# Optimization experiments

Hardware: AMD Instinct MI355X
Metric: run time of the kernel (lower is better)

## Reference

```python
import jax, jax.numpy as jnp
import numpy as np

N_ADAPTERS = 8
RANK = 64  # per-adapter LoRA rank (uniform here; ragged in general)
SCALINGS = np.full((N_ADAPTERS,), 2.0, dtype=np.float32)  # alpha / r


def setup_inputs() -> dict:
    key = jax.random.key(0)
    k1, k2, k3, k4, k5 = jax.random.split(key, 5)
    T, DIN, DOUT = 8192, 4096, 4096
    total_rank = N_ADAPTERS * RANK
    x = jax.random.normal(k1, (T, DIN), dtype=jnp.float32)
    lora_A = jax.random.normal(k2, (total_rank, DIN), dtype=jnp.float32) * 0.02
    lora_B = jax.random.normal(k3, (total_rank, DOUT), dtype=jnp.float32) * 0.02
    base_output = jax.random.normal(k4, (T, DOUT), dtype=jnp.float32)
    adapter_ids = jax.random.randint(k5, (T,), 0, N_ADAPTERS, dtype=jnp.int64)
    return {"x": x, "lora_A": lora_A, "lora_B": lora_B,
            "base_output": base_output, "adapter_ids": adapter_ids}


def reference(x, lora_A, lora_B, base_output, adapter_ids):
    """Multi-adapter LoRA: out = base + scaling[a] * (x @ A_a.T) @ B_a per token.

    base_slice covers the full out_features here, so the LoRA delta is added
    to the whole base_output. Loop is over the small fixed adapter set.
    """
    lora_out = jnp.zeros_like(base_output)
    for a in range(N_ADAPTERS):
        A_a = lora_A[a * RANK:(a + 1) * RANK]  # [R, DIN]
        B_a = lora_B[a * RANK:(a + 1) * RANK]  # [R, DOUT]
        xa = x @ A_a.T                          # [T, R]
        mask = (adapter_ids == a).astype(x.dtype)[:, None]
        lora_out = lora_out + SCALINGS[a] * ((xa * mask) @ B_a)
    return base_output + lora_out
```

## Files before the change

### kernel.cpp

```cpp
#include <hip/hip_runtime.h>
#include <hip/hip_bf16.h>

#define T_TOK 8192
#define DIN   4096
#define DOUT  4096
#define RANK  64
#define NAD   8
#define TS    32
#define MAXTILES 264
#define TOTR  (NAD*RANK)
#define KSPLIT 4
#define KCH   (DIN / KSPLIT)
#define NT    (KCH / 64)
#define DSPLIT 8
#define DCH   (DOUT / DSPLIT)
#define NS    (DCH / 64)

typedef __bf16 bf16x8 __attribute__((ext_vector_type(8)));
typedef __bf16 bf16x4 __attribute__((ext_vector_type(4)));
typedef float  f32x4  __attribute__((ext_vector_type(4)));

#define WS_CURSORS 0
#define WS_NTILES  64
#define WS_FLAG    128
#define WS_TINFO   256
#define WS_PERM    4096
#define WS_XA      0x10000
#define WS_ABF     0x110000
#define WS_BT      0x510000
#define WS_XAP     0x910000
#define WS_END     (0x910000 + (size_t)KSPLIT * T_TOK * RANK * 4)

__device__ __forceinline__ void gll16(const void* g, void* l) {
  __builtin_amdgcn_global_load_lds(
      (const __attribute__((address_space(1))) unsigned int*)g,
      (__attribute__((address_space(3))) unsigned int*)l, 16, 0, 0);
}

__global__ __launch_bounds__(1024) void hist_prep(const int* __restrict__ ids,
    int* __restrict__ cursors, int* __restrict__ ntilesp,
    int* __restrict__ flagp, int* __restrict__ tinfo) {
  __shared__ int cnt[NAD];
  __shared__ int s_ofs[NAD], s_tbase[NAD + 1];
  __shared__ int s_is64;
  int tid = threadIdx.x, lane = tid & 63;
  if (tid < NAD) cnt[tid] = 0;
  if (tid == 0) s_is64 = 1;
  __syncthreads();
  int any = 0;
  for (int i = tid; i < T_TOK; i += 1024)
    if (i & 1) any |= ids[i];
  if (any) s_is64 = 0;
  __syncthreads();
  int is64 = s_is64;
  int loc[NAD];
#pragma unroll
  for (int a = 0; a < NAD; ++a) loc[a] = 0;
  for (int t = tid; t < T_TOK; t += 1024) {
    int id = (is64 ? ids[2 * t] : ids[t]) & 7;
#pragma unroll
    for (int a = 0; a < NAD; ++a) {
      unsigned long long m = __ballot(id == a);
      if (lane == 0) loc[a] += __popcll(m);
    }
  }
  if (lane == 0) {
#pragma unroll
    for (int a = 0; a < NAD; ++a) if (loc[a]) atomicAdd(&cnt[a], loc[a]);
  }
  __syncthreads();
  if (tid == 0) {
    *flagp = is64;
    int ofs = 0, tb = 0;
    for (int a = 0; a < NAD; ++a) {
      s_ofs[a] = ofs; cursors[a] = ofs;
      s_tbase[a] = tb;
      ofs += cnt[a];
      tb += (cnt[a] + TS - 1) / TS;
    }
    s_tbase[NAD] = tb;
    *ntilesp = tb;
  }
  __syncthreads();
  int ntt = s_tbase[NAD];
  for (int e = tid; e < ntt; e += 1024) {
    int a = 0;
    while (e >= s_tbase[a + 1]) ++a;
    int t0 = (e - s_tbase[a]) * TS;
    int c = cnt[a];
    tinfo[e * 3 + 0] = a;
    tinfo[e * 3 + 1] = s_ofs[a] + t0;
    tinfo[e * 3 + 2] = (c - t0 < TS) ? (c - t0) : TS;
  }
}

__global__ __launch_bounds__(256) void scatter_k(const int* __restrict__ ids,
    const int* __restrict__ flagp, int* __restrict__ cursors, int* __restrict__ perm) {
  int t = blockIdx.x * 256 + threadIdx.x;
  int lane = threadIdx.x & 63;
  int id = ((*flagp) ? ids[2 * t] : ids[t]) & 7;
  unsigned long long lt = (1ull << lane) - 1ull;
#pragma unroll
  for (int a = 0; a < NAD; ++a) {
    unsigned long long m = __ballot(id == a);
    if (m) {
      int leader = __ffsll((long long)m) - 1;
      int base_a = 0;
      if (lane == leader) base_a = atomicAdd(&cursors[a], __popcll(m));
      base_a = __shfl(base_a, leader, 64);
      if (id == a) perm[base_a + __popcll(m & lt)] = t;
    }
  }
}

__global__ __launch_bounds__(256) void prep_ab(const float* __restrict__ A,
    __bf16* __restrict__ Abf, const float* __restrict__ B, __bf16* __restrict__ Bt) {
  if (blockIdx.x < 2048) {
    int i = blockIdx.x * 256 + threadIdx.x;
    float4 v = ((const float4*)A)[i];
    bf16x4 o = { (__bf16)v.x, (__bf16)v.y, (__bf16)v.z, (__bf16)v.w };
    ((bf16x4*)Abf)[i] = o;
  } else {
    __shared__ float t[64][65];
    int idx = blockIdx.x - 2048;
    int rb = idx & 7, db = idx >> 3;
    int tid = threadIdx.x;
    int c = tid & 63, q = tid >> 6;
#pragma unroll
    for (int i = 0; i < 16; ++i) {
      int r = i * 4 + q;
      t[r][c] = B[(size_t)(rb * 64 + r) * DOUT + db * 64 + c];
    }
    __syncthreads();
#pragma unroll
    for (int i = 0; i < 16; ++i) {
      int d = i * 4 + q;
      Bt[(size_t)(db * 64 + d) * TOTR + rb * 64 + c] = (__bf16)t[c][d];
    }
  }
}

#define CVT8(lo, hi) { (__bf16)lo.x, (__bf16)lo.y, (__bf16)lo.z, (__bf16)lo.w, \
                       (__bf16)hi.x, (__bf16)hi.y, (__bf16)hi.z, (__bf16)hi.w }

__global__ __launch_bounds__(512) void stage1s(const float* __restrict__ x,
    const __bf16* __restrict__ Abf, const int* __restrict__ tinfo,
    const int* __restrict__ ntilesp, const int* __restrict__ perm,
    float* __restrict__ xap) {
  __shared__ char lds[4][16384];
  int b = blockIdx.x;
  if (b >= *ntilesp) return;
  int ks = blockIdx.y;
  int a = tinfo[b * 3], start = tinfo[b * 3 + 1], nv = tinfo[b * 3 + 2];
  int tid = threadIdx.x, lane = tid & 63, wv = tid >> 6;

  int xr = wv * 4 + (lane >> 4);
  int xtok = (xr < nv) ? perm[start + xr] : perm[start];
  int xinner = ((lane & 15) * 16) ^ ((xr & 7) << 4);
  const char* xsrc = (const char*)(x + (size_t)xtok * DIN + ks * KCH) + xinner;
  int ar = wv * 8 + (lane >> 3);
  int ainner = ((lane & 7) * 16) ^ ((ar & 7) << 4);
  const char* asrc = (const char*)(Abf + (size_t)(a * RANK + ar) * DIN + ks * KCH) + ainner;

  int l16 = lane & 15, lq = lane >> 4;
  int rb = wv & 1, cb = wv >> 1;
  int xrow = rb * 16 + l16;
  int arow = cb * 16 + l16;
  int swx = (xrow & 7) << 4;
  int swa = (arow & 7) << 4;

  f32x4 acc = {0.f, 0.f, 0.f, 0.f};

#pragma unroll
  for (int p = 0; p < 3; ++p) {
    gll16(xsrc + (size_t)p * 256, &lds[p][wv * 1024]);
    gll16(asrc + (size_t)p * 128, &lds[p][8192 + wv * 1024]);
  }

  for (int t = 0; t < NT; ++t) {
    if (t < NT - 2)       asm volatile("s_waitcnt vmcnt(4)" ::: "memory");
    else if (t == NT - 2) asm volatile("s_waitcnt vmcnt(2)" ::: "memory");
    else                  asm volatile("s_waitcnt vmcnt(0)" ::: "memory");
    __builtin_amdgcn_s_barrier();
    asm volatile("" ::: "memory");
    if (t + 3 < NT) {
      char* nbuf = lds[(t + 3) & 3];
      gll16(xsrc + (size_t)(t + 3) * 256, nbuf + wv * 1024);
      gll16(asrc + (size_t)(t + 3) * 128, nbuf + 8192 + wv * 1024);
    }
    const char* cbuf = lds[t & 3];
#pragma unroll
    for (int m = 0; m < 2; ++m) {
      f32x4 xv0 = *(const f32x4*)(cbuf + xrow * 256 + ((m * 128 + lq * 32) ^ swx));
      f32x4 xv1 = *(const f32x4*)(cbuf + xrow * 256 + ((m * 128 + lq * 32 + 16) ^ swx));
      bf16x8 xf = { (__bf16)xv0[0], (__bf16)xv0[1], (__bf16)xv0[2], (__bf16)xv0[3],
                    (__bf16)xv1[0], (__bf16)xv1[1], (__bf16)xv1[2], (__bf16)xv1[3] };
      bf16x8 af = *(const bf16x8*)(cbuf + 8192 + arow * 128 + ((m * 64 + lq * 16) ^ swa));
      acc = __builtin_amdgcn_mfma_f32_16x16x32_bf16(xf, af, acc, 0, 0, 0);
    }
    asm volatile("" ::: "memory");
  }

  float* xo = xap + (size_t)ks * T_TOK * RANK;
#pragma unroll
  for (int j = 0; j < 4; ++j) {
    int tr = rb * 16 + lq * 4 + j;
    if (tr < nv) {
      int tk = perm[start + tr];
      xo[(size_t)tk * RANK + cb * 16 + l16] = acc[j];
    }
  }
}

__global__ __launch_bounds__(256) void reduce_xa(const float* __restrict__ xap,
                                                 __bf16* __restrict__ xa) {
  int i = blockIdx.x * 256 + threadIdx.x;
  const float4* p = (const float4*)xap;
  float4 s = p[i];
#pragma unroll
  for (int ks = 1; ks < KSPLIT; ++ks) {
    float4 q = p[(size_t)ks * (T_TOK * RANK / 4) + i];
    s.x += q.x; s.y += q.y; s.z += q.z; s.w += q.w;
  }
  bf16x4 o = { (__bf16)s.x, (__bf16)s.y, (__bf16)s.z, (__bf16)s.w };
  ((bf16x4*)xa)[i] = o;
}

__global__ __launch_bounds__(512) void stage1f(const float* __restrict__ x,
    const __bf16* __restrict__ Abf, const int* __restrict__ tinfo,
    const int* __restrict__ ntilesp, const int* __restrict__ perm,
    __bf16* __restrict__ xa) {
  int b = blockIdx.x;
  if (b >= *ntilesp) return;
  int a = tinfo[b * 3], start = tinfo[b * 3 + 1], nv = tinfo[b * 3 + 2];
  int tid = threadIdx.x, lane = tid & 63, w = tid >> 6;
  int rb = w & 1, cb = w >> 1;
  int l16 = lane & 15, lq = lane >> 4;
  int trow = rb * 16 + l16;
  int tok = (trow < nv) ? perm[start + trow] : 0;
  const float*  xrow = x + (size_t)tok * DIN + lq * 8;
  const __bf16* arow = Abf + (size_t)(a * RANK + cb * 16 + l16) * DIN + lq * 8;
  f32x4 acc = {0.f, 0.f, 0.f, 0.f};
#pragma unroll 4
  for (int k0 = 0; k0 < DIN; k0 += 32) {
    float4 v0 = *(const float4*)(xrow + k0);
    float4 v1 = *(const float4*)(xrow + k0 + 4);
    bf16x8 af = CVT8(v0, v1);
    bf16x8 bfr = *(const bf16x8*)(arow + k0);
    acc = __builtin_amdgcn_mfma_f32_16x16x32_bf16(af, bfr, acc, 0, 0, 0);
  }
#pragma unroll
  for (int j = 0; j < 4; ++j) {
    int tr = rb * 16 + lq * 4 + j;
    if (tr < nv) {
      int tk = perm[start + tr];
      xa[(size_t)tk * RANK + cb * 16 + l16] = (__bf16)acc[j];
    }
  }
}

__global__ __launch_bounds__(512) void stage2(const __bf16* __restrict__ xa,
    const __bf16* __restrict__ Bt, const float* __restrict__ base,
    const int* __restrict__ tinfo, const int* __restrict__ ntilesp,
    const int* __restrict__ perm, float* __restrict__ out) {
  __shared__ char lds[4][16384];
  int b = blockIdx.y;
  if (b >= *ntilesp) return;
  int a = tinfo[b * 3], start = tinfo[b * 3 + 1], nv = tinfo[b * 3 + 2];
  int tid = threadIdx.x, lane = tid & 63, wv = tid >> 6;
  int dblk = blockIdx.x * DCH;

  int brow = wv * 4 + (lane >> 4);
  int btok = (brow < nv) ? perm[start + brow] : perm[start];
  int binner = ((lane & 15) * 16) ^ ((brow & 7) << 4);
  const char* bsrc = (const char*)(base + (size_t)btok * DOUT + dblk) + binner;
  int trow = wv * 8 + (lane >> 3);
  int tinner = ((lane & 7) * 16) ^ ((trow & 7) << 4);
  const char* tsrc = (const char*)(Bt + (size_t)(dblk + trow) * TOTR + a * RANK) + tinner;

  int tb = wv & 1, dg = wv >> 1;
  int l16 = lane & 15, lq = lane >> 4;
  int tIdx = tb * 16 + l16;
  bool valid = tIdx < nv;
  int token = valid ? perm[start + tIdx] : perm[start];

  const __bf16* xrow = xa + (size_t)token * RANK + lq * 8;
  bf16x8 xv0 = *(const bf16x8*)(xrow);
  bf16x8 xv1 = *(const bf16x8*)(xrow + 32);

  float* orow = out + (size_t)token * DOUT + dblk + dg * 16 + lq * 4;

  int btrow = dg * 16 + l16;
  int btoff0 = btrow * 128 + ((lq * 16) ^ ((btrow & 7) << 4));
  int btoff1 = btrow * 128 + ((lq * 16 + 64) ^ ((btrow & 7) << 4));
  int bsoff  = tIdx * 256 + ((dg * 64 + lq * 16) ^ ((tIdx & 7) << 4));

  f32x4 res[NS];

  asm volatile("" ::: "memory");
#pragma unroll
  for (int p = 0; p < 3; ++p) {
    gll16(bsrc + (size_t)p * 256,   &lds[p][wv * 1024]);
    gll16(tsrc + (size_t)p * 65536, &lds[p][8192 + wv * 1024]);
  }

#pragma unroll
  for (int t = 0; t < NS; ++t) {
    if (t < NS - 2)       asm volatile("s_waitcnt vmcnt(4)" ::: "memory");
    else if (t == NS - 2) asm volatile("s_waitcnt vmcnt(2)" ::: "memory");
    else                  asm volatile("s_waitcnt vmcnt(0)" ::: "memory");
    __builtin_amdgcn_s_barrier();
    asm volatile("" ::: "memory");
    if (t + 3 < NS) {
      char* nbuf = lds[(t + 3) & 3];
      gll16(bsrc + (size_t)(t + 3) * 256,   nbuf + wv * 1024);
      gll16(tsrc + (size_t)(t + 3) * 65536, nbuf + 8192 + wv * 1024);
    }
    const char* cbuf = lds[t & 3];
    bf16x8 bf0 = *(const bf16x8*)(cbuf + 8192 + btoff0);
    bf16x8 bf1 = *(const bf16x8*)(cbuf + 8192 + btoff1);
    f32x4  bs  = *(const f32x4*)(cbuf + bsoff);
    f32x4 z = {0.f, 0.f, 0.f, 0.f};
    z = __builtin_amdgcn_mfma_f32_16x16x32_bf16(bf0, xv0, z, 0, 0, 0);
    z = __builtin_amdgcn_mfma_f32_16x16x32_bf16(bf1, xv1, z, 0, 0, 0);
    res[t][0] = bs[0] + 2.0f * z[0];
    res[t][1] = bs[1] + 2.0f * z[1];
    res[t][2] = bs[2] + 2.0f * z[2];
    res[t][3] = bs[3] + 2.0f * z[3];
    asm volatile("" ::: "memory");
  }

  if (valid) {
#pragma unroll
    for (int t = 0; t < NS; ++t)
      *(float4*)(orow + t * 64) = *(const float4*)&res[t];
  }
}

extern "C" void kernel_launch(void* const* d_in, const int* in_sizes, int n_in,
                              void* d_out, int out_size, void* d_ws, size_t ws_size,
                              hipStream_t stream) {
  const float* x   = (const float*)d_in[0];
  const float* A   = (const float*)d_in[1];
  const float* B   = (const float*)d_in[2];
  const float* bas = (const float*)d_in[3];
  const int*   ids = (const int*)d_in[4];
  float* out = (float*)d_out;
  char* ws = (char*)d_ws;
  int* cursors = (int*)(ws + WS_CURSORS);
  int* ntiles  = (int*)(ws + WS_NTILES);
  int* flag    = (int*)(ws + WS_FLAG);
  int* tinfo   = (int*)(ws + WS_TINFO);
  int* perm    = (int*)(ws + WS_PERM);
  __bf16* xa   = (__bf16*)(ws + WS_XA);
  __bf16* Abf  = (__bf16*)(ws + WS_ABF);
  __bf16* Bt   = (__bf16*)(ws + WS_BT);
  float*  xap  = (float*)(ws + WS_XAP);

  hist_prep<<<1, 1024, 0, stream>>>(ids, cursors, ntiles, flag, tinfo);
  scatter_k<<<T_TOK / 256, 256, 0, stream>>>(ids, flag, cursors, perm);
  prep_ab<<<2048 + 512, 256, 0, stream>>>(A, Abf, B, Bt);
  if (ws_size >= WS_END) {
    stage1s<<<dim3(MAXTILES, KSPLIT), 512, 0, stream>>>(x, Abf, tinfo, ntiles, perm, xap);
    reduce_xa<<<(T_TOK * RANK / 4) / 256, 256, 0, stream>>>(xap, xa);
  } else {
    stage1f<<<MAXTILES, 512, 0, stream>>>(x, Abf, tinfo, ntiles, perm, xa);
  }
  stage2<<<dim3(DSPLIT, MAXTILES), 512, 0, stream>>>(xa, Bt, bas, tinfo, ntiles, perm, out);
}
```

Before: 149.1 us.

## Double token tile size, double-buffer LDS, and fuse scatter into histogram kernel

Token tiles grow from 32 to 64 rows so each block reuses its loaded A slice (stage1) and B^T slice (stage2) across twice as many tokens, roughly halving adapter-weight traffic per token. The LDS pipeline drops from a 4-deep to a 2-deep buffer with an extra barrier each step, and each wave now computes two MFMA output tiles. Stage2's DOUT split doubles to keep the grid size up. The separate scatter kernel is folded into the single-block histogram kernel using LDS cursors, saving one launch but running the scatter on one workgroup.

```diff
diff --git a/kernel.cpp b/kernel.cpp
--- a/kernel.cpp
+++ b/kernel.cpp
@@ -6,13 +6,13 @@
 #define DOUT  4096
 #define RANK  64
 #define NAD   8
-#define TS    32
-#define MAXTILES 264
+#define TS    64
+#define MAXTILES 135
 #define TOTR  (NAD*RANK)
 #define KSPLIT 4
 #define KCH   (DIN / KSPLIT)
 #define NT    (KCH / 64)
-#define DSPLIT 8
+#define DSPLIT 16
 #define DCH   (DOUT / DSPLIT)
 #define NS    (DCH / 64)
 
@@ -20,9 +20,7 @@
 typedef __bf16 bf16x4 __attribute__((ext_vector_type(4)));
 typedef float  f32x4  __attribute__((ext_vector_type(4)));
 
-#define WS_CURSORS 0
 #define WS_NTILES  64
-#define WS_FLAG    128
 #define WS_TINFO   256
 #define WS_PERM    4096
 #define WS_XA      0x10000
@@ -38,10 +36,8 @@
 }
 
 __global__ __launch_bounds__(1024) void hist_prep(const int* __restrict__ ids,
-    int* __restrict__ cursors, int* __restrict__ ntilesp,
-    int* __restrict__ flagp, int* __restrict__ tinfo) {
-  __shared__ int cnt[NAD];
-  __shared__ int s_ofs[NAD], s_tbase[NAD + 1];
+    int* __restrict__ ntilesp, int* __restrict__ tinfo, int* __restrict__ perm) {
+  __shared__ int cnt[NAD], s_ofs[NAD], s_cur[NAD], s_tbase[NAD + 1];
   __shared__ int s_is64;
   int tid = threadIdx.x, lane = tid & 63;
   if (tid < NAD) cnt[tid] = 0;
@@ -70,10 +66,9 @@
   }
   __syncthreads();
   if (tid == 0) {
-    *flagp = is64;
     int ofs = 0, tb = 0;
     for (int a = 0; a < NAD; ++a) {
-      s_ofs[a] = ofs; cursors[a] = ofs;
+      s_ofs[a] = ofs;
       s_tbase[a] = tb;
       ofs += cnt[a];
       tb += (cnt[a] + TS - 1) / TS;
@@ -82,6 +77,7 @@
     *ntilesp = tb;
   }
   __syncthreads();
+  if (tid < NAD) s_cur[tid] = s_ofs[tid];
   int ntt = s_tbase[NAD];
   for (int e = tid; e < ntt; e += 1024) {
     int a = 0;
@@ -92,23 +88,20 @@
     tinfo[e * 3 + 1] = s_ofs[a] + t0;
     tinfo[e * 3 + 2] = (c - t0 < TS) ? (c - t0) : TS;
   }
-}
-
-__global__ __launch_bounds__(256) void scatter_k(const int* __restrict__ ids,
-    const int* __restrict__ flagp, int* __restrict__ cursors, int* __restrict__ perm) {
-  int t = blockIdx.x * 256 + threadIdx.x;
-  int lane = threadIdx.x & 63;
-  int id = ((*flagp) ? ids[2 * t] : ids[t]) & 7;
+  __syncthreads();
   unsigned long long lt = (1ull << lane) - 1ull;
-#pragma unroll
-  for (int a = 0; a < NAD; ++a) {
-    unsigned long long m = __ballot(id == a);
-    if (m) {
-      int leader = __ffsll((long long)m) - 1;
-      int base_a = 0;
-      if (lane == leader) base_a = atomicAdd(&cursors[a], __popcll(m));
-      base_a = __shfl(base_a, leader, 64);
-      if (id == a) perm[base_a + __popcll(m & lt)] = t;
+  for (int t = tid; t < T_TOK; t += 1024) {
+    int id = (is64 ? ids[2 * t] : ids[t]) & 7;
+#pragma unroll
+    for (int a = 0; a < NAD; ++a) {
+      unsigned long long m = __ballot(id == a);
+      if (m) {
+        int leader = __ffsll((long long)m) - 1;
+        int base_a = 0;
+        if (lane == leader) base_a = atomicAdd(&s_cur[a], __popcll(m));
+        base_a = __shfl(base_a, leader, 64);
+        if (id == a) perm[base_a + __popcll(m & lt)] = t;
+      }
     }
   }
 }
@@ -140,74 +133,81 @@
   }
 }
 
-#define CVT8(lo, hi) { (__bf16)lo.x, (__bf16)lo.y, (__bf16)lo.z, (__bf16)lo.w, \
-                       (__bf16)hi.x, (__bf16)hi.y, (__bf16)hi.z, (__bf16)hi.w }
+#define CVT8(lo, hi) { (__bf16)lo[0], (__bf16)lo[1], (__bf16)lo[2], (__bf16)lo[3], \
+                       (__bf16)hi[0], (__bf16)hi[1], (__bf16)hi[2], (__bf16)hi[3] }
 
 __global__ __launch_bounds__(512) void stage1s(const float* __restrict__ x,
     const __bf16* __restrict__ Abf, const int* __restrict__ tinfo,
     const int* __restrict__ ntilesp, const int* __restrict__ perm,
     float* __restrict__ xap) {
-  __shared__ char lds[4][16384];
+  __shared__ char lds[2][24576];
   int b = blockIdx.x;
   if (b >= *ntilesp) return;
   int ks = blockIdx.y;
   int a = tinfo[b * 3], start = tinfo[b * 3 + 1], nv = tinfo[b * 3 + 2];
   int tid = threadIdx.x, lane = tid & 63, wv = tid >> 6;
 
-  int xr = wv * 4 + (lane >> 4);
-  int xtok = (xr < nv) ? perm[start + xr] : perm[start];
-  int xinner = ((lane & 15) * 16) ^ ((xr & 7) << 4);
-  const char* xsrc = (const char*)(x + (size_t)xtok * DIN + ks * KCH) + xinner;
+  int xr0 = wv * 4 + (lane >> 4);
+  int xr1 = xr0 + 32;
+  int xt0 = (xr0 < nv) ? perm[start + xr0] : perm[start];
+  int xt1 = (xr1 < nv) ? perm[start + xr1] : perm[start];
+  const char* xs0 = (const char*)(x + (size_t)xt0 * DIN + ks * KCH)
+                    + (((lane & 15) * 16) ^ ((xr0 & 7) << 4));
+  const char* xs1 = (const char*)(x + (size_t)xt1 * DIN + ks * KCH)
+                    + (((lane & 15) * 16) ^ ((xr1 & 7) << 4));
   int ar = wv * 8 + (lane >> 3);
-  int ainner = ((lane & 7) * 16) ^ ((ar & 7) << 4);
-  const char* asrc = (const char*)(Abf + (size_t)(a * RANK + ar) * DIN + ks * KCH) + ainner;
+  const char* as = (const char*)(Abf + (size_t)(a * RANK + ar) * DIN + ks * KCH)
+                   + (((lane & 7) * 16) ^ ((ar & 7) << 4));
 
   int l16 = lane & 15, lq = lane >> 4;
-  int rb = wv & 1, cb = wv >> 1;
-  int xrow = rb * 16 + l16;
-  int arow = cb * 16 + l16;
+  int tq = wv & 3, rh = wv >> 2;
+  int xrow = tq * 16 + l16;
   int swx = (xrow & 7) << 4;
-  int swa = (arow & 7) << 4;
-
-  f32x4 acc = {0.f, 0.f, 0.f, 0.f};
-
-#pragma unroll
-  for (int p = 0; p < 3; ++p) {
-    gll16(xsrc + (size_t)p * 256, &lds[p][wv * 1024]);
-    gll16(asrc + (size_t)p * 128, &lds[p][8192 + wv * 1024]);
-  }
+  int arow0 = rh * 32 + l16;
+  int arow1 = arow0 + 16;
+  int swa = (arow0 & 7) << 4;
+
+  f32x4 acc0 = {0.f, 0.f, 0.f, 0.f}, acc1 = {0.f, 0.f, 0.f, 0.f};
+
+  gll16(xs0, &lds[0][wv * 1024]);
+  gll16(xs1, &lds[0][8192 + wv * 1024]);
+  gll16(as,  &lds[0][16384 + wv * 1024]);
 
   for (int t = 0; t < NT; ++t) {
-    if (t < NT - 2)       asm volatile("s_waitcnt vmcnt(4)" ::: "memory");
-    else if (t == NT - 2) asm volatile("s_waitcnt vmcnt(2)" ::: "memory");
-    else                  asm volatile("s_waitcnt vmcnt(0)" ::: "memory");
+    if (t + 1 < NT) {
+      char* nb = lds[(t + 1) & 1];
+      gll16(xs0 + (size_t)(t + 1) * 256, nb + wv * 1024);
+      gll16(xs1 + (size_t)(t + 1) * 256, nb + 8192 + wv * 1024);
+      gll16(as  + (size_t)(t + 1) * 128, nb + 16384 + wv * 1024);
+      asm volatile("s_waitcnt vmcnt(3)" ::: "memory");
+    } else {
+      asm volatile("s_waitcnt vmcnt(0)" ::: "memory");
+    }
     __builtin_amdgcn_s_barrier();
     asm volatile("" ::: "memory");
-    if (t + 3 < NT) {
-      char* nbuf = lds[(t + 3) & 3];
-      gll16(xsrc + (size_t)(t + 3) * 256, nbuf + wv * 1024);
-      gll16(asrc + (size_t)(t + 3) * 128, nbuf + 8192 + wv * 1024);
-    }
-    const char* cbuf = lds[t & 3];
+    const char* cb = lds[t & 1];
 #pragma unroll
     for (int m = 0; m < 2; ++m) {
-      f32x4 xv0 = *(const f32x4*)(cbuf + xrow * 256 + ((m * 128 + lq * 32) ^ swx));
-      f32x4 xv1 = *(const f32x4*)(cbuf + xrow * 256 + ((m * 128 + lq * 32 + 16) ^ swx));
-      bf16x8 xf = { (__bf16)xv0[0], (__bf16)xv0[1], (__bf16)xv0[2], (__bf16)xv0[3],
-                    (__bf16)xv1[0], (__bf16)xv1[1], (__bf16)xv1[2], (__bf16)xv1[3] };
-      bf16x8 af = *(const bf16x8*)(cbuf + 8192 + arow * 128 + ((m * 64 + lq * 16) ^ swa));
-      acc = __builtin_amdgcn_mfma_f32_16x16x32_bf16(xf, af, acc, 0, 0, 0);
+      f32x4 xv0 = *(const f32x4*)(cb + xrow * 256 + ((m * 128 + lq * 32) ^ swx));
+      f32x4 xv1 = *(const f32x4*)(cb + xrow * 256 + ((m * 128 + lq * 32 + 16) ^ swx));
+      bf16x8 xf = CVT8(xv0, xv1);
+      bf16x8 a0 = *(const bf16x8*)(cb + 16384 + arow0 * 128 + ((m * 64 + lq * 16) ^ swa));
+      bf16x8 a1 = *(const bf16x8*)(cb + 16384 + arow1 * 128 + ((m * 64 + lq * 16) ^ swa));
+      acc0 = __builtin_amdgcn_mfma_f32_16x16x32_bf16(xf, a0, acc0, 0, 0, 0);
+      acc1 = __builtin_amdgcn_mfma_f32_16x16x32_bf16(xf, a1, acc1, 0, 0, 0);
     }
     asm volatile("" ::: "memory");
+    __builtin_amdgcn_s_barrier();
   }
 
   float* xo = xap + (size_t)ks * T_TOK * RANK;
 #pragma unroll
   for (int j = 0; j < 4; ++j) {
-    int tr = rb * 16 + lq * 4 + j;
+    int tr = tq * 16 + lq * 4 + j;
     if (tr < nv) {
       int tk = perm[start + tr];
-      xo[(size_t)tk * RANK + cb * 16 + l16] = acc[j];
+      xo[(size_t)tk * RANK + rh * 32 + l16]      = acc0[j];
+      xo[(size_t)tk * RANK + rh * 32 + 16 + l16] = acc1[j];
     }
   }
 }
@@ -233,28 +233,32 @@
   int b = blockIdx.x;
   if (b >= *ntilesp) return;
   int a = tinfo[b * 3], start = tinfo[b * 3 + 1], nv = tinfo[b * 3 + 2];
-  int tid = threadIdx.x, lane = tid & 63, w = tid >> 6;
-  int rb = w & 1, cb = w >> 1;
+  int tid = threadIdx.x, lane = tid & 63, wv = tid >> 6;
   int l16 = lane & 15, lq = lane >> 4;
-  int trow = rb * 16 + l16;
-  int tok = (trow < nv) ? perm[start + trow] : 0;
-  const float*  xrow = x + (size_t)tok * DIN + lq * 8;
-  const __bf16* arow = Abf + (size_t)(a * RANK + cb * 16 + l16) * DIN + lq * 8;
-  f32x4 acc = {0.f, 0.f, 0.f, 0.f};
+  int tq = wv & 3, rh = wv >> 2;
+  int trow = tq * 16 + l16;
+  int tok = (trow < nv) ? perm[start + trow] : perm[start];
+  const float*  xr = x + (size_t)tok * DIN + lq * 8;
+  const __bf16* a0p = Abf + (size_t)(a * RANK + rh * 32 + l16) * DIN + lq * 8;
+  const __bf16* a1p = a0p + (size_t)16 * DIN;
+  f32x4 acc0 = {0.f, 0.f, 0.f, 0.f}, acc1 = {0.f, 0.f, 0.f, 0.f};
 #pragma unroll 4
   for (int k0 = 0; k0 < DIN; k0 += 32) {
-    float4 v0 = *(const float4*)(xrow + k0);
-    float4 v1 = *(const float4*)(xrow + k0 + 4);
-    bf16x8 af = CVT8(v0, v1);
-    bf16x8 bfr = *(const bf16x8*)(arow + k0);
-    acc = __builtin_amdgcn_mfma_f32_16x16x32_bf16(af, bfr, acc, 0, 0, 0);
+    f32x4 v0 = *(const f32x4*)(xr + k0);
+    f32x4 v1 = *(const f32x4*)(xr + k0 + 4);
+    bf16x8 xf = CVT8(v0, v1);
+    bf16x8 f0 = *(const bf16x8*)(a0p + k0);
+    bf16x8 f1 = *(const bf16x8*)(a1p + k0);
+    acc0 = __builtin_amdgcn_mfma_f32_16x16x32_bf16(xf, f0, acc0, 0, 0, 0);
+    acc1 = __builtin_amdgcn_mfma_f32_16x16x32_bf16(xf, f1, acc1, 0, 0, 0);
   }
 #pragma unroll
   for (int j = 0; j < 4; ++j) {
-    int tr = rb * 16 + lq * 4 + j;
+    int tr = tq * 16 + lq * 4 + j;
     if (tr < nv) {
       int tk = perm[start + tr];
-      xa[(size_t)tk * RANK + cb * 16 + l16] = (__bf16)acc[j];
+      xa[(size_t)tk * RANK + rh * 32 + l16]      = (__bf16)acc0[j];
+      xa[(size_t)tk * RANK + rh * 32 + 16 + l16] = (__bf16)acc1[j];
     }
   }
 }
@@ -263,24 +267,27 @@
     const __bf16* __restrict__ Bt, const float* __restrict__ base,
     const int* __restrict__ tinfo, const int* __restrict__ ntilesp,
     const int* __restrict__ perm, float* __restrict__ out) {
-  __shared__ char lds[4][16384];
+  __shared__ char lds[2][24576];
   int b = blockIdx.y;
   if (b >= *ntilesp) return;
   int a = tinfo[b * 3], start = tinfo[b * 3 + 1], nv = tinfo[b * 3 + 2];
   int tid = threadIdx.x, lane = tid & 63, wv = tid >> 6;
   int dblk = blockIdx.x * DCH;
 
-  int brow = wv * 4 + (lane >> 4);
-  int btok = (brow < nv) ? perm[start + brow] : perm[start];
-  int binner = ((lane & 15) * 16) ^ ((brow & 7) << 4);
-  const char* bsrc = (const char*)(base + (size_t)btok * DOUT + dblk) + binner;
-  int trow = wv * 8 + (lane >> 3);
-  int tinner = ((lane & 7) * 16) ^ ((trow & 7) << 4);
-  const char* tsrc = (const char*)(Bt + (size_t)(dblk + trow) * TOTR + a * RANK) + tinner;
-
-  int tb = wv & 1, dg = wv >> 1;
+  int br0 = wv * 4 + (lane >> 4), br1 = br0 + 32;
+  int bt0 = (br0 < nv) ? perm[start + br0] : perm[start];
+  int bt1 = (br1 < nv) ? perm[start + br1] : perm[start];
+  const char* bs0 = (const char*)(base + (size_t)bt0 * DOUT + dblk)
+                    + (((lane & 15) * 16) ^ ((br0 & 7) << 4));
+  const char* bs1 = (const char*)(base + (size_t)bt1 * DOUT + dblk)
+                    + (((lane & 15) * 16) ^ ((br1 & 7) << 4));
+  int trw = wv * 8 + (lane >> 3);
+  const char* ts = (const char*)(Bt + (size_t)(dblk + trw) * TOTR + a * RANK)
+                   + (((lane & 7) * 16) ^ ((trw & 7) << 4));
+
   int l16 = lane & 15, lq = lane >> 4;
-  int tIdx = tb * 16 + l16;
+  int tq = wv & 3, dh = wv >> 2;
+  int tIdx = tq * 16 + l16;
   bool valid = tIdx < nv;
   int token = valid ? perm[start + tIdx] : perm[start];
 
@@ -288,52 +295,56 @@
   bf16x8 xv0 = *(const bf16x8*)(xrow);
   bf16x8 xv1 = *(const bf16x8*)(xrow + 32);
 
-  float* orow = out + (size_t)token * DOUT + dblk + dg * 16 + lq * 4;
-
-  int btrow = dg * 16 + l16;
-  int btoff0 = btrow * 128 + ((lq * 16) ^ ((btrow & 7) << 4));
-  int btoff1 = btrow * 128 + ((lq * 16 + 64) ^ ((btrow & 7) << 4));
-  int bsoff  = tIdx * 256 + ((dg * 64 + lq * 16) ^ ((tIdx & 7) << 4));
-
-  f32x4 res[NS];
+  int swt = (tIdx & 7) << 4;
+  int btr0 = dh * 32 + l16, btr1 = btr0 + 16;
+  int swb = (btr0 & 7) << 4;
+
+  f32x4 res[NS][2];
 
   asm volatile("" ::: "memory");
-#pragma unroll
-  for (int p = 0; p < 3; ++p) {
-    gll16(bsrc + (size_t)p * 256,   &lds[p][wv * 1024]);
-    gll16(tsrc + (size_t)p * 65536, &lds[p][8192 + wv * 1024]);
-  }
+  gll16(bs0, &lds[0][wv * 1024]);
+  gll16(bs1, &lds[0][8192 + wv * 1024]);
+  gll16(ts,  &lds[0][16384 + wv * 1024]);
 
 #pragma unroll
   for (int t = 0; t < NS; ++t) {
-    if (t < NS - 2)       asm volatile("s_waitcnt vmcnt(4)" ::: "memory");
-    else if (t == NS - 2) asm volatile("s_waitcnt vmcnt(2)" ::: "memory");
-    else                  asm volatile("s_waitcnt vmcnt(0)" ::: "memory");
+    if (t + 1 < NS) {
+      char* nb = lds[(t + 1) & 1];
+      gll16(bs0 + (size_t)(t + 1) * 256,   nb + wv * 1024);
+      gll16(bs1 + (size_t)(t + 1) * 256,   nb + 8192 + wv * 1024);
+      gll16(ts  + (size_t)(t + 1) * 65536, nb + 16384 + wv * 1024);
+      asm volatile("s_waitcnt vmcnt(3)" ::: "memory");
+    } else {
+      asm volatile("s_waitcnt vmcnt(0)" ::: "memory");
+    }
     __builtin_amdgcn_s_barrier();
     asm volatile("" ::: "memory");
-    if (t + 3 < NS) {
-      char* nbuf = lds[(t + 3) & 3];
-      gll16(bsrc + (size_t)(t + 3) * 256,   nbuf + wv * 1024);
-      gll16(tsrc + (size_t)(t + 3) * 65536, nbuf + 8192 + wv * 1024);
-    }
-    const char* cbuf = lds[t & 3];
-    bf16x8 bf0 = *(const bf16x8*)(cbuf + 8192 + btoff0);
-    bf16x8 bf1 = *(const bf16x8*)(cbuf + 8192 + btoff1);
-    f32x4  bs  = *(const f32x4*)(cbuf + bsoff);
-    f32x4 z = {0.f, 0.f, 0.f, 0.f};
-    z = __builtin_amdgcn_mfma_f32_16x16x32_bf16(bf0, xv0, z, 0, 0, 0);
-    z = __builtin_amdgcn_mfma_f32_16x16x32_bf16(bf1, xv1, z, 0, 0, 0);
-    res[t][0] = bs[0] + 2.0f * z[0];
-    res[t][1] = bs[1] + 2.0f * z[1];
-    res[t][2] = bs[2] + 2.0f * z[2];
-    res[t][3] = bs[3] + 2.0f * z[3];
+    const char* cb = lds[t & 1];
+#pragma unroll
+    for (int dt = 0; dt < 2; ++dt) {
+      int btr = dt ? btr1 : btr0;
+      bf16x8 bf0 = *(const bf16x8*)(cb + 16384 + btr * 128 + ((lq * 16) ^ swb));
+      bf16x8 bf1 = *(const bf16x8*)(cb + 16384 + btr * 128 + ((lq * 16 + 64) ^ swb));
+      f32x4  bs  = *(const f32x4*)(cb + tIdx * 256 + ((dh * 128 + dt * 64 + lq * 16) ^ swt));
+      f32x4 z = {0.f, 0.f, 0.f, 0.f};
+      z = __builtin_amdgcn_mfma_f32_16x16x32_bf16(bf0, xv0, z, 0, 0, 0);
+      z = __builtin_amdgcn_mfma_f32_16x16x32_bf16(bf1, xv1, z, 0, 0, 0);
+      res[t][dt][0] = bs[0] + 2.0f * z[0];
+      res[t][dt][1] = bs[1] + 2.0f * z[1];
+      res[t][dt][2] = bs[2] + 2.0f * z[2];
+      res[t][dt][3] = bs[3] + 2.0f * z[3];
+    }
     asm volatile("" ::: "memory");
+    __builtin_amdgcn_s_barrier();
   }
 
   if (valid) {
+    float* orow = out + (size_t)token * DOUT + dblk;
 #pragma unroll
     for (int t = 0; t < NS; ++t)
-      *(float4*)(orow + t * 64) = *(const float4*)&res[t];
+#pragma unroll
+      for (int dt = 0; dt < 2; ++dt)
+        *(float4*)(orow + t * 64 + dh * 32 + dt * 16 + lq * 4) = *(const float4*)&res[t][dt];
   }
 }
 
@@ -347,9 +358,7 @@
   const int*   ids = (const int*)d_in[4];
   float* out = (float*)d_out;
   char* ws = (char*)d_ws;
-  int* cursors = (int*)(ws + WS_CURSORS);
   int* ntiles  = (int*)(ws + WS_NTILES);
-  int* flag    = (int*)(ws + WS_FLAG);
   int* tinfo   = (int*)(ws + WS_TINFO);
   int* perm    = (int*)(ws + WS_PERM);
   __bf16* xa   = (__bf16*)(ws + WS_XA);
@@ -357,8 +366,7 @@
   __bf16* Bt   = (__bf16*)(ws + WS_BT);
   float*  xap  = (float*)(ws + WS_XAP);
 
-  hist_prep<<<1, 1024, 0, stream>>>(ids, cursors, ntiles, flag, tinfo);
-  scatter_k<<<T_TOK / 256, 256, 0, stream>>>(ids, flag, cursors, perm);
+  hist_prep<<<1, 1024, 0, stream>>>(ids, ntiles, tinfo, perm);
   prep_ab<<<2048 + 512, 256, 0, stream>>>(A, Abf, B, Bt);
   if (ws_size >= WS_END) {
     stage1s<<<dim3(MAXTILES, KSPLIT), 512, 0, stream>>>(x, Abf, tinfo, ntiles, perm, xap);
```

After: 145.4 us. 2.5% less time.
